# Performance work log

Hardware: AMD Instinct MI355X
Metric: run time of the kernel (lower is better)

Reference implementation:

```python
import jax, jax.numpy as jnp
import numpy as np

HIDDEN = 64
N_CLASSES = 10
N_NODES = 100000
N_EDGES = 1600000
N_GRAPHS = 64


def setup_inputs() -> dict:
    key = jax.random.key(0)
    ks = jax.random.split(key, 16)
    src = jax.random.randint(ks[0], (N_EDGES,), 0, N_NODES, dtype=jnp.int32)
    dst = jax.random.randint(ks[1], (N_EDGES,), 0, N_NODES, dtype=jnp.int32)
    graph_ids = jnp.sort(jax.random.randint(ks[2], (N_NODES,), 0, N_GRAPHS, dtype=jnp.int32))
    def glorot(k, shape):
        fan_in, fan_out = shape
        lim = np.sqrt(6.0 / (fan_in + fan_out)).astype(np.float32)
        return jax.random.uniform(k, shape, jnp.float32, -lim, lim)
    return {
        "src": src, "dst": dst, "graph_ids": graph_ids, "n_graphs": N_GRAPHS,
        "W1": glorot(ks[3], (1, HIDDEN)),      "b1": jnp.zeros((HIDDEN,), jnp.float32),
        "W2": glorot(ks[4], (HIDDEN, HIDDEN)), "b2": jnp.zeros((HIDDEN,), jnp.float32),
        "W3": glorot(ks[5], (HIDDEN, HIDDEN)), "b3": jnp.zeros((HIDDEN,), jnp.float32),
        "W4": glorot(ks[6], (HIDDEN, HIDDEN)), "b4": jnp.zeros((HIDDEN,), jnp.float32),
        "Wc": glorot(ks[7], (HIDDEN, N_CLASSES)), "bc": jnp.zeros((N_CLASSES,), jnp.float32),
    }


def reference(src, dst, graph_ids, n_graphs, W1, b1, W2, b2, W3, b3, W4, b4, Wc, bc):
    N = graph_ids.shape[0]
    ones_e = jnp.ones(src.shape, jnp.float32)
    in_deg = jax.ops.segment_sum(ones_e, dst, num_segments=N)    # [N]
    out_deg = jax.ops.segment_sum(ones_e, src, num_segments=N)   # [N]
    # DGL GraphConv norm='both': clamp degrees to >=1 (allow_zero_in_degree)
    norm_src = jnp.maximum(out_deg, 1.0)[:, None] ** -0.5        # [N,1]
    norm_dst = jnp.maximum(in_deg, 1.0)[:, None] ** -0.5         # [N,1]

    def graph_conv(h, W, b):
        h = h * norm_src
        agg = jax.ops.segment_sum(h[src], dst, num_segments=N)
        agg = agg * norm_dst
        return agg @ W + b

    h = in_deg[:, None]                                          # node feature = in-degree
    h = jax.nn.relu(graph_conv(h, W1, b1))
    h = jax.nn.relu(graph_conv(h, W2, b2))
    h = jax.nn.relu(graph_conv(h, W3, b3))
    h = jax.nn.relu(graph_conv(h, W4, b4))

    # dgl.mean_nodes: per-graph mean pooling over batched graph
    counts = jax.ops.segment_sum(jnp.ones((N,), jnp.float32), graph_ids, num_segments=n_graphs)
    hg = jax.ops.segment_sum(h, graph_ids, num_segments=n_graphs) / jnp.maximum(counts, 1.0)[:, None]
    return hg, hg @ Wc + bc
```

## Files before the change

### kernel.cpp

```cpp
#include <hip/hip_runtime.h>
#include <hip/hip_bf16.h>


__global__ void deg_kernel(const int* __restrict__ src, const int* __restrict__ dst,
                           int* __restrict__ in_deg, int* __restrict__ out_deg, int E) {
    int stride = gridDim.x * blockDim.x;
    int E4 = E >> 2;
    const int4* src4 = (const int4*)src;
    const int4* dst4 = (const int4*)dst;
    for (int e = blockIdx.x * blockDim.x + threadIdx.x; e < E4; e += stride) {
        int4 s = src4[e], d = dst4[e];
        atomicAdd(&in_deg[d.x], 1); atomicAdd(&in_deg[d.y], 1);
        atomicAdd(&in_deg[d.z], 1); atomicAdd(&in_deg[d.w], 1);
        atomicAdd(&out_deg[s.x], 1); atomicAdd(&out_deg[s.y], 1);
        atomicAdd(&out_deg[s.z], 1); atomicAdd(&out_deg[s.w], 1);
    }
    int tid = blockIdx.x * blockDim.x + threadIdx.x;
    if (tid < (E & 3)) {
        int e = (E4 << 2) + tid;
        atomicAdd(&in_deg[dst[e]], 1);
        atomicAdd(&out_deg[src[e]], 1);
    }
}

__global__ void norm_kernel(const int* __restrict__ in_deg, const int* __restrict__ out_deg,
                            float* __restrict__ norm_src, float* __restrict__ norm_dst,
                            float* __restrict__ xs, int N) {
    int n = blockIdx.x * blockDim.x + threadIdx.x;
    if (n < N) {
        float id = (float)in_deg[n];
        float od = (float)out_deg[n];
        float ns = rsqrtf(fmaxf(od, 1.0f));
        norm_src[n] = ns;
        norm_dst[n] = rsqrtf(fmaxf(id, 1.0f));
        xs[n] = id * ns;
    }
}

__global__ void scan_reduce(const int* __restrict__ vals, int* __restrict__ block_sums, int N) {
    int t = threadIdx.x, b = blockIdx.x;
    int base = b * 1024 + t * 4;
    int s = 0;
    #pragma unroll
    for (int k = 0; k < 4; ++k) { int i = base + k; if (i < N) s += vals[i]; }
    for (int d = 32; d > 0; d >>= 1) s += __shfl_down(s, d, 64);
    __shared__ int wsum[4];
    if ((t & 63) == 0) wsum[t >> 6] = s;
    __syncthreads();
    if (t == 0) block_sums[b] = wsum[0] + wsum[1] + wsum[2] + wsum[3];
}

__global__ void scan_top(const int* __restrict__ block_sums, int* __restrict__ block_offs,
                         int NB, int* __restrict__ row_ptr, int N) {
    __shared__ int ts[1024];
    int t = threadIdx.x;
    int s = (t < NB) ? block_sums[t] : 0;
    ts[t] = s;
    __syncthreads();
    for (int d = 1; d < 1024; d <<= 1) {
        int x = (t >= d) ? ts[t - d] : 0;
        __syncthreads();
        ts[t] += x;
        __syncthreads();
    }
    block_offs[t] = ts[t] - s;
    if (t == 1023) row_ptr[N] = ts[1023];
}

__global__ void scan_apply(const int* __restrict__ vals, const int* __restrict__ block_offs,
                           int* __restrict__ row_ptr, int* __restrict__ cursor, int N) {
    __shared__ int ts[256];
    int t = threadIdx.x, b = blockIdx.x;
    int base = b * 1024 + t * 4;
    int v[4]; int s = 0;
    #pragma unroll
    for (int k = 0; k < 4; ++k) { int i = base + k; v[k] = (i < N) ? vals[i] : 0; s += v[k]; }
    ts[t] = s;
    __syncthreads();
    for (int d = 1; d < 256; d <<= 1) {
        int x = (t >= d) ? ts[t - d] : 0;
        __syncthreads();
        ts[t] += x;
        __syncthreads();
    }
    int ex = block_offs[b] + ts[t] - s;
    #pragma unroll
    for (int k = 0; k < 4; ++k) {
        int i = base + k;
        if (i < N) { row_ptr[i] = ex; cursor[i] = ex; }
        ex += v[k];
    }
}

__global__ void fill_kernel(const int* __restrict__ src, const int* __restrict__ dst,
                            int* __restrict__ cursor, int* __restrict__ csr_src, int E, int N) {
    int slice = blockIdx.x & 7;
    int bs    = blockIdx.x >> 3;
    int nbs   = gridDim.x >> 3;
    int lo = (int)(((long long)slice * N) / 8);
    int hi = (slice == 7) ? N : (int)(((long long)(slice + 1) * N) / 8);
    int stride = nbs * blockDim.x;
    int E4 = E >> 2;
    const int4* src4 = (const int4*)src;
    const int4* dst4 = (const int4*)dst;
    for (int e = bs * blockDim.x + threadIdx.x; e < E4; e += stride) {
        int4 s = src4[e], d = dst4[e];
        if (d.x >= lo && d.x < hi) csr_src[atomicAdd(&cursor[d.x], 1)] = s.x;
        if (d.y >= lo && d.y < hi) csr_src[atomicAdd(&cursor[d.y], 1)] = s.y;
        if (d.z >= lo && d.z < hi) csr_src[atomicAdd(&cursor[d.z], 1)] = s.z;
        if (d.w >= lo && d.w < hi) csr_src[atomicAdd(&cursor[d.w], 1)] = s.w;
    }
    if (slice == 0 && bs == 0) {
        int tid = threadIdx.x;
        if (tid < (E & 3)) {
            int e = (E4 << 2) + tid;
            csr_src[atomicAdd(&cursor[dst[e]], 1)] = src[e];
        }
    }
}

__global__ void agg1_kernel(const int* __restrict__ row_ptr, const int* __restrict__ csr_src,
                            const float* __restrict__ xs, const float* __restrict__ norm_dst,
                            float* __restrict__ a_buf, int N) {
    int n = blockIdx.x * blockDim.x + threadIdx.x;
    if (n < N) {
        int s0 = row_ptr[n], s1 = row_ptr[n + 1];
        float a = 0.0f;
        for (int i = s0; i < s1; ++i) a += xs[csr_src[i]];
        a_buf[n] = a * norm_dst[n];
    }
}

__global__ void dense1_kernel(const float* __restrict__ a_buf, const float* __restrict__ norm_src,
                              const float* __restrict__ W1, const float* __restrict__ b1,
                              __hip_bfloat16* __restrict__ out, int N) {
    int stride = gridDim.x * blockDim.x;
    int total = N * 64;
    for (int i = blockIdx.x * blockDim.x + threadIdx.x; i < total; i += stride) {
        int n = i >> 6, j = i & 63;
        float y = fmaxf(fmaf(a_buf[n], W1[j], b1[j]), 0.0f);
        out[i] = __float2bfloat16(y * norm_src[n]);
    }
}

__global__ void conv_fused(const int* __restrict__ row_ptr, const int* __restrict__ csr_src,
                           const uint4* __restrict__ xb, const float* __restrict__ norm_dst,
                           const float* __restrict__ norm_src, const float* __restrict__ W,
                           const float* __restrict__ b, float* __restrict__ out_f32,
                           __hip_bfloat16* __restrict__ out_bf,
                           int N, int apply_src, int store_bf16) {
    __shared__ float Wsh[64 * 64];
    for (int i = threadIdx.x; i < 64 * 64; i += blockDim.x) Wsh[i] = W[i];
    __syncthreads();
    int lane = threadIdx.x & 63;
    int slot = lane >> 3;
    int q    = lane & 7;
    int grp  = threadIdx.x >> 6;
    int gpb  = blockDim.x >> 6;
    int gw   = blockIdx.x * gpb + grp;
    int nw   = gridDim.x * gpb;
    float bj = b[lane];
    for (int n = gw; n < N; n += nw) {
        int s0 = row_ptr[n], s1 = row_ptr[n + 1];
        float f0 = 0.f, f1 = 0.f, f2 = 0.f, f3 = 0.f,
              f4 = 0.f, f5 = 0.f, f6 = 0.f, f7 = 0.f;
        for (int i = s0 + slot; i < s1; i += 16) {
            int sA = csr_src[i];
            int i2 = i + 8;
            uint4 uA = xb[(size_t)sA * 8 + q];
            uint4 uB = make_uint4(0u, 0u, 0u, 0u);
            if (i2 < s1) {
                int sB = csr_src[i2];
                uB = xb[(size_t)sB * 8 + q];
            }
            f0 += __uint_as_float(uA.x << 16) + __uint_as_float(uB.x << 16);
            f1 += __uint_as_float(uA.x & 0xFFFF0000u) + __uint_as_float(uB.x & 0xFFFF0000u);
            f2 += __uint_as_float(uA.y << 16) + __uint_as_float(uB.y << 16);
            f3 += __uint_as_float(uA.y & 0xFFFF0000u) + __uint_as_float(uB.y & 0xFFFF0000u);
            f4 += __uint_as_float(uA.z << 16) + __uint_as_float(uB.z << 16);
            f5 += __uint_as_float(uA.z & 0xFFFF0000u) + __uint_as_float(uB.z & 0xFFFF0000u);
            f6 += __uint_as_float(uA.w << 16) + __uint_as_float(uB.w << 16);
            f7 += __uint_as_float(uA.w & 0xFFFF0000u) + __uint_as_float(uB.w & 0xFFFF0000u);
        }
        #pragma unroll
        for (int m = 8; m <= 32; m <<= 1) {
            f0 += __shfl_xor(f0, m, 64); f1 += __shfl_xor(f1, m, 64);
            f2 += __shfl_xor(f2, m, 64); f3 += __shfl_xor(f3, m, 64);
            f4 += __shfl_xor(f4, m, 64); f5 += __shfl_xor(f5, m, 64);
            f6 += __shfl_xor(f6, m, 64); f7 += __shfl_xor(f7, m, 64);
        }
        float nd = norm_dst[n];
        f0 *= nd; f1 *= nd; f2 *= nd; f3 *= nd;
        f4 *= nd; f5 *= nd; f6 *= nd; f7 *= nd;
        float y = bj;
        #pragma unroll
        for (int k = 0; k < 64; ++k) {
            float comp = (k & 7) == 0 ? f0 : (k & 7) == 1 ? f1 : (k & 7) == 2 ? f2 :
                         (k & 7) == 3 ? f3 : (k & 7) == 4 ? f4 : (k & 7) == 5 ? f5 :
                         (k & 7) == 6 ? f6 : f7;
            float vk = __shfl(comp, k >> 3, 64);
            y = fmaf(vk, Wsh[k * 64 + lane], y);
        }
        y = fmaxf(y, 0.0f);
        if (apply_src) y *= norm_src[n];
        if (store_bf16) out_bf[(size_t)n * 64 + lane] = __float2bfloat16(y);
        else            out_f32[(size_t)n * 64 + lane] = y;
    }
}

__global__ void pool_partial(const float* __restrict__ h, const int* __restrict__ gid, int N,
                             float* __restrict__ partial) {
    int g  = blockIdx.x >> 2;
    int qt = blockIdx.x & 3;
    int lo = 0, hi = N;
    while (lo < hi) { int mid = (lo + hi) >> 1; if (gid[mid] < g) lo = mid + 1; else hi = mid; }
    int start = lo;
    hi = N;
    while (lo < hi) { int mid = (lo + hi) >> 1; if (gid[mid] < g + 1) lo = mid + 1; else hi = mid; }
    int end = lo;
    int cnt = end - start;
    int qlo = start + (int)(((long long)cnt * qt) / 4);
    int qhi = start + (int)(((long long)cnt * (qt + 1)) / 4);

    int lane = threadIdx.x & 63;
    int grp  = threadIdx.x >> 6;
    float acc = 0.0f;
    for (int n = qlo + grp; n < qhi; n += 4) acc += h[(size_t)n * 64 + lane];

    __shared__ float sh[4][64];
    sh[grp][lane] = acc;
    __syncthreads();
    if (threadIdx.x < 64)
        partial[(size_t)blockIdx.x * 64 + lane] =
            sh[0][lane] + sh[1][lane] + sh[2][lane] + sh[3][lane];
}

__global__ void pool_final(const float* __restrict__ partial, const int* __restrict__ gid, int N,
                           const float* __restrict__ Wc, const float* __restrict__ bc,
                           float* __restrict__ out, int n_graphs) {
    int g = blockIdx.x;
    int lo = 0, hi = N;
    while (lo < hi) { int mid = (lo + hi) >> 1; if (gid[mid] < g) lo = mid + 1; else hi = mid; }
    int start = lo;
    hi = N;
    while (lo < hi) { int mid = (lo + hi) >> 1; if (gid[mid] < g + 1) lo = mid + 1; else hi = mid; }
    int cnt = lo - start;

    int lane = threadIdx.x;
    __shared__ float hrow[64];
    float s = partial[(size_t)(g * 4 + 0) * 64 + lane] + partial[(size_t)(g * 4 + 1) * 64 + lane]
            + partial[(size_t)(g * 4 + 2) * 64 + lane] + partial[(size_t)(g * 4 + 3) * 64 + lane];
    float m = s / fmaxf((float)cnt, 1.0f);
    hrow[lane] = m;
    out[(size_t)g * 64 + lane] = m;
    __syncthreads();
    if (lane < 10) {
        float acc2 = bc[lane];
        #pragma unroll
        for (int j = 0; j < 64; ++j) acc2 = fmaf(hrow[j], Wc[j * 10 + lane], acc2);
        out[(size_t)n_graphs * 64 + (size_t)g * 10 + lane] = acc2;
    }
}

extern "C" void kernel_launch(void* const* d_in, const int* in_sizes, int n_in,
                              void* d_out, int out_size, void* d_ws, size_t ws_size,
                              hipStream_t stream) {
    const int*   src = (const int*)d_in[0];
    const int*   dst = (const int*)d_in[1];
    const int*   gid = (const int*)d_in[2];
    const float* W1  = (const float*)d_in[4];
    const float* b1  = (const float*)d_in[5];
    const float* W2  = (const float*)d_in[6];
    const float* b2  = (const float*)d_in[7];
    const float* W3  = (const float*)d_in[8];
    const float* b3  = (const float*)d_in[9];
    const float* W4  = (const float*)d_in[10];
    const float* b4  = (const float*)d_in[11];
    const float* Wc  = (const float*)d_in[12];
    const float* bc  = (const float*)d_in[13];

    int E  = in_sizes[0];
    int N  = in_sizes[2];
    int ng = out_size / 74;

    int* in_deg_i   = (int*)d_ws;
    int* out_deg_i  = in_deg_i + N;
    int* row_ptr    = out_deg_i + N;
    int* cursor     = row_ptr + N + 1;
    int* csr_src    = cursor + N;
    int* block_sums = csr_src + E;
    int* block_offs = block_sums + 1024;
    float* norm_src = (float*)(block_offs + 1024);
    float* norm_dst = norm_src + N;
    float* xs       = norm_dst + N;
    float* a_buf    = xs + N;
    float* bufA     = (float*)(((uintptr_t)(a_buf + N) + 15) & ~(uintptr_t)15);
    __hip_bfloat16* hb1 = (__hip_bfloat16*)(bufA + 64 * (size_t)N);
    __hip_bfloat16* hb2 = hb1 + 64 * (size_t)N;
    float* partial  = (float*)(hb2 + 64 * (size_t)N);

    float* out_f = (float*)d_out;

    int NB = (N + 1023) / 1024;

    hipMemsetAsync(in_deg_i, 0, 2 * (size_t)N * sizeof(int), stream);
    deg_kernel<<<2048, 256, 0, stream>>>(src, dst, in_deg_i, out_deg_i, E);
    norm_kernel<<<(N + 255) / 256, 256, 0, stream>>>(in_deg_i, out_deg_i, norm_src, norm_dst, xs, N);

    scan_reduce<<<NB, 256, 0, stream>>>(in_deg_i, block_sums, N);
    scan_top<<<1, 1024, 0, stream>>>(block_sums, block_offs, NB, row_ptr, N);
    scan_apply<<<NB, 256, 0, stream>>>(in_deg_i, block_offs, row_ptr, cursor, N);
    fill_kernel<<<2048, 256, 0, stream>>>(src, dst, cursor, csr_src, E, N);

    agg1_kernel<<<(N + 255) / 256, 256, 0, stream>>>(row_ptr, csr_src, xs, norm_dst, a_buf, N);
    dense1_kernel<<<2048, 256, 0, stream>>>(a_buf, norm_src, W1, b1, hb1, N);

    conv_fused<<<2048, 256, 0, stream>>>(row_ptr, csr_src, (const uint4*)hb1, norm_dst, norm_src,
                                         W2, b2, nullptr, hb2, N, 1, 1);
    conv_fused<<<2048, 256, 0, stream>>>(row_ptr, csr_src, (const uint4*)hb2, norm_dst, norm_src,
                                         W3, b3, nullptr, hb1, N, 1, 1);
    conv_fused<<<2048, 256, 0, stream>>>(row_ptr, csr_src, (const uint4*)hb1, norm_dst, norm_src,
                                         W4, b4, bufA, nullptr, N, 0, 0);

    pool_partial<<<ng * 4, 256, 0, stream>>>(bufA, gid, N, partial);
    pool_final<<<ng, 64, 0, stream>>>(partial, gid, N, Wc, bc, out_f, ng);
}
```

Before: 703.0 us.

## Replace global-atomic degree counting with sliced shared-memory histograms

Degree counting now uses per-block LDS histograms, one per node slice and edge partition, instead of global atomics. The partial counts are written to a workspace and summed in the norm kernel, which also writes in_deg. This removes the memset and contended global atomics. In exchange, every block re-reads its edge partition to filter by slice, so the edge list is read many times over and the launch has only 128 blocks.

```diff
diff --git a/kernel.cpp b/kernel.cpp
--- a/kernel.cpp
+++ b/kernel.cpp
@@ -2,39 +2,76 @@
 #include <hip/hip_bf16.h>
 
 
-__global__ void deg_kernel(const int* __restrict__ src, const int* __restrict__ dst,
-                           int* __restrict__ in_deg, int* __restrict__ out_deg, int E) {
-    int stride = gridDim.x * blockDim.x;
+#define HSLICES 16
+#define HBPS    8
+#define HCAP    6272
+
+__global__ __launch_bounds__(1024) void hist_kernel(const int* __restrict__ src,
+                                                    const int* __restrict__ dst,
+                                                    int* __restrict__ partials, int E, int N) {
+    __shared__ int lin[HCAP];
+    __shared__ int lout[HCAP];
+    int s  = blockIdx.x >> 3;
+    int bp = blockIdx.x & 7;
+    int lo  = (int)(((long long)s * N) / HSLICES);
+    int hi  = (int)(((long long)(s + 1) * N) / HSLICES);
+    int rng = hi - lo;
+    for (int i = threadIdx.x; i < HCAP; i += 1024) { lin[i] = 0; lout[i] = 0; }
+    __syncthreads();
+
     int E4 = E >> 2;
+    int P4 = (E4 + HBPS - 1) / HBPS;
+    int p0 = bp * P4;
+    int p1 = p0 + P4; if (p1 > E4) p1 = E4;
     const int4* src4 = (const int4*)src;
     const int4* dst4 = (const int4*)dst;
-    for (int e = blockIdx.x * blockDim.x + threadIdx.x; e < E4; e += stride) {
-        int4 s = src4[e], d = dst4[e];
-        atomicAdd(&in_deg[d.x], 1); atomicAdd(&in_deg[d.y], 1);
-        atomicAdd(&in_deg[d.z], 1); atomicAdd(&in_deg[d.w], 1);
-        atomicAdd(&out_deg[s.x], 1); atomicAdd(&out_deg[s.y], 1);
-        atomicAdd(&out_deg[s.z], 1); atomicAdd(&out_deg[s.w], 1);
-    }
-    int tid = blockIdx.x * blockDim.x + threadIdx.x;
-    if (tid < (E & 3)) {
-        int e = (E4 << 2) + tid;
-        atomicAdd(&in_deg[dst[e]], 1);
-        atomicAdd(&out_deg[src[e]], 1);
-    }
-}
-
-__global__ void norm_kernel(const int* __restrict__ in_deg, const int* __restrict__ out_deg,
+    for (int e = p0 + threadIdx.x; e < p1; e += 1024) {
+        int4 sv = src4[e], dv = dst4[e];
+        if ((unsigned)(dv.x - lo) < (unsigned)rng) atomicAdd(&lin[dv.x - lo], 1);
+        if ((unsigned)(dv.y - lo) < (unsigned)rng) atomicAdd(&lin[dv.y - lo], 1);
+        if ((unsigned)(dv.z - lo) < (unsigned)rng) atomicAdd(&lin[dv.z - lo], 1);
+        if ((unsigned)(dv.w - lo) < (unsigned)rng) atomicAdd(&lin[dv.w - lo], 1);
+        if ((unsigned)(sv.x - lo) < (unsigned)rng) atomicAdd(&lout[sv.x - lo], 1);
+        if ((unsigned)(sv.y - lo) < (unsigned)rng) atomicAdd(&lout[sv.y - lo], 1);
+        if ((unsigned)(sv.z - lo) < (unsigned)rng) atomicAdd(&lout[sv.z - lo], 1);
+        if ((unsigned)(sv.w - lo) < (unsigned)rng) atomicAdd(&lout[sv.w - lo], 1);
+    }
+    if (bp == HBPS - 1) {
+        for (int e = (E4 << 2) + threadIdx.x; e < E; e += 1024) {
+            int d = dst[e], sc = src[e];
+            if ((unsigned)(d - lo) < (unsigned)rng) atomicAdd(&lin[d - lo], 1);
+            if ((unsigned)(sc - lo) < (unsigned)rng) atomicAdd(&lout[sc - lo], 1);
+        }
+    }
+    __syncthreads();
+    int base = (s * HBPS + bp) * (2 * HCAP);
+    for (int i = threadIdx.x; i < rng; i += 1024) {
+        partials[base + i]        = lin[i];
+        partials[base + HCAP + i] = lout[i];
+    }
+}
+
+__global__ void norm_kernel(const int* __restrict__ partials, int* __restrict__ in_deg,
                             float* __restrict__ norm_src, float* __restrict__ norm_dst,
                             float* __restrict__ xs, int N) {
     int n = blockIdx.x * blockDim.x + threadIdx.x;
-    if (n < N) {
-        float id = (float)in_deg[n];
-        float od = (float)out_deg[n];
-        float ns = rsqrtf(fmaxf(od, 1.0f));
-        norm_src[n] = ns;
-        norm_dst[n] = rsqrtf(fmaxf(id, 1.0f));
-        xs[n] = id * ns;
-    }
+    if (n >= N) return;
+    int s  = (int)(((long long)n * HSLICES) / N);
+    int lo = (int)(((long long)s * N) / HSLICES);
+    int l  = n - lo;
+    int id = 0, od = 0;
+    #pragma unroll
+    for (int bp = 0; bp < HBPS; ++bp) {
+        int base = (s * HBPS + bp) * (2 * HCAP);
+        id += partials[base + l];
+        od += partials[base + HCAP + l];
+    }
+    in_deg[n] = id;
+    float idf = (float)id, odf = (float)od;
+    float ns = rsqrtf(fmaxf(odf, 1.0f));
+    norm_src[n] = ns;
+    norm_dst[n] = rsqrtf(fmaxf(idf, 1.0f));
+    xs[n] = idf * ns;
 }
 
 __global__ void scan_reduce(const int* __restrict__ vals, int* __restrict__ block_sums, int N) {
@@ -284,8 +321,7 @@
     int ng = out_size / 74;
 
     int* in_deg_i   = (int*)d_ws;
-    int* out_deg_i  = in_deg_i + N;
-    int* row_ptr    = out_deg_i + N;
+    int* row_ptr    = in_deg_i + N;
     int* cursor     = row_ptr + N + 1;
     int* csr_src    = cursor + N;
     int* block_sums = csr_src + E;
@@ -298,14 +334,14 @@
     __hip_bfloat16* hb1 = (__hip_bfloat16*)(bufA + 64 * (size_t)N);
     __hip_bfloat16* hb2 = hb1 + 64 * (size_t)N;
     float* partial  = (float*)(hb2 + 64 * (size_t)N);
+    int* hpart      = (int*)bufA;
 
     float* out_f = (float*)d_out;
 
     int NB = (N + 1023) / 1024;
 
-    hipMemsetAsync(in_deg_i, 0, 2 * (size_t)N * sizeof(int), stream);
-    deg_kernel<<<2048, 256, 0, stream>>>(src, dst, in_deg_i, out_deg_i, E);
-    norm_kernel<<<(N + 255) / 256, 256, 0, stream>>>(in_deg_i, out_deg_i, norm_src, norm_dst, xs, N);
+    hist_kernel<<<HSLICES * HBPS, 1024, 0, stream>>>(src, dst, hpart, E, N);
+    norm_kernel<<<(N + 255) / 256, 256, 0, stream>>>(hpart, in_deg_i, norm_src, norm_dst, xs, N);
 
     scan_reduce<<<NB, 256, 0, stream>>>(in_deg_i, block_sums, N);
     scan_top<<<1, 1024, 0, stream>>>(block_sums, block_offs, NB, row_ptr, N);
```

Measured after the change: 601.3 us. 1.17x faster.
